# Performance work log

Measured on AMD Instinct MI355X. Metric: run time of the kernel, lower is better.

Reference implementation:

```python
import jax, jax.numpy as jnp
import numpy as np

N_KERNELS = 11
INV_SQRT_2PI = 1.0 / np.sqrt(2.0 * 3.141592653589793)


def kernel_mus(n_kernels):
    l_mu = [1.0]
    if n_kernels == 1:
        return l_mu
    bin_size = 2.0 / (n_kernels - 1)
    l_mu.append(1 - bin_size / 2)
    for i in range(1, n_kernels - 1):
        l_mu.append(l_mu[i] - bin_size)
    return l_mu


def kernel_sigmas(n_kernels):
    bin_size = 2.0 / (n_kernels - 1)
    l_sigma = [0.0001]
    if n_kernels == 1:
        return l_sigma
    l_sigma += [0.5 * bin_size] * (n_kernels - 1)
    return l_sigma


MU = jnp.asarray(kernel_mus(N_KERNELS), dtype=jnp.float32)        # [K]
SIGMA = jnp.asarray(kernel_sigmas(N_KERNELS), dtype=jnp.float32)  # [K]


def setup_inputs() -> dict:
    key = jax.random.key(0)
    k1, k2, k3, k4 = jax.random.split(key, 4)
    B, Q, D, V, E = 512, 32, 256, 32000, 128
    return {
        "query_tokens": jax.random.randint(k1, (B, Q), 0, V),
        "doc_tokens": jax.random.randint(k2, (B, D), 0, V),
        "embedding": jax.random.normal(k3, (V, E), dtype=jnp.float32),
        "fc_weight": jax.random.normal(k4, (1, N_KERNELS), dtype=jnp.float32) * 0.3,
    }


def reference(query_tokens, doc_tokens, embedding, fc_weight):
    # embedding lookup + L2 normalization along feature dim
    q_emb = embedding[query_tokens]                                  # [B,Q,E]
    d_emb = embedding[doc_tokens]                                    # [B,D,E]
    q_n = q_emb / jnp.linalg.norm(q_emb, axis=-1, keepdims=True)
    d_n = d_emb / jnp.linalg.norm(d_emb, axis=-1, keepdims=True)

    # cosine similarity translation matrix [B,Q,D]
    tm = jnp.einsum("bqe,bde->bqd", q_n, d_n)

    # Gaussian kernel responses [B,Q,D,K] (vectorized over kernels)
    diff = tm[..., None] - MU                                        # [B,Q,D,K]
    kmat = jnp.exp(-(diff * diff) / (2.0 * SIGMA * SIGMA)) * INV_SQRT_2PI

    # masking: pad/OOV tokens (id 0) masked out
    q_mask = (query_tokens > 0).astype(jnp.float32)                  # [B,Q]
    d_mask = (doc_tokens > 0).astype(jnp.float32)                    # [B,D]
    kmat = kmat * q_mask[:, :, None, None] * d_mask[:, None, :, None]

    # kernel pooling: sum over doc, log, masked sum over query
    per_kernel_query = jnp.sum(kmat, axis=2)                         # [B,Q,K]
    log_pool = jnp.log(jnp.clip(per_kernel_query, 1e-10)) * q_mask[:, :, None]
    per_kernel = jnp.sum(log_pool, axis=1)                           # [B,K]

    # final linear (no bias) -> score per (query, document) pair
    return jnp.squeeze(per_kernel @ fc_weight.T, axis=-1)            # [B]
```

## Files before the change

### kernel.cpp

```cpp
#include <hip/hip_runtime.h>
#include <hip/hip_bf16.h>

#define EDIM  128
#define QN    32
#define DN    256
#define NK    11

typedef __attribute__((ext_vector_type(8))) short bf16x8;
typedef __attribute__((ext_vector_type(4))) float f32x4;

#define EXP2F(x) __builtin_amdgcn_exp2f(x)

template <int CTRL>
static __device__ inline float dpp_add(float x) {
    int y = __builtin_amdgcn_update_dpp(0, __float_as_int(x), CTRL, 0xF, 0xF, true);
    return x + __int_as_float(y);
}
static __device__ inline float sum16(float x) {
    x = dpp_add<0xB1>(x);
    x = dpp_add<0x4E>(x);
    x = dpp_add<0x124>(x);
    x = dpp_add<0x128>(x);
    return x;
}

static __device__ inline int swz(int r, int c) { return c ^ ((r & 7) << 4); }

static __device__ inline bf16x8 pack8(float4 a, float4 b) {
    union { bf16x8 v; __hip_bfloat16 h[8]; } u;
    u.h[0] = __float2bfloat16(a.x); u.h[1] = __float2bfloat16(a.y);
    u.h[2] = __float2bfloat16(a.z); u.h[3] = __float2bfloat16(a.w);
    u.h[4] = __float2bfloat16(b.x); u.h[5] = __float2bfloat16(b.y);
    u.h[6] = __float2bfloat16(b.z); u.h[7] = __float2bfloat16(b.w);
    return u.v;
}
static __device__ inline float sumsq8(float4 a, float4 b) {
    float s = a.x * a.x + a.y * a.y + a.z * a.z + a.w * a.w;
    s = fmaf(b.x, b.x, s); s = fmaf(b.y, b.y, s);
    s = fmaf(b.z, b.z, s); s = fmaf(b.w, b.w, s);
    return s;
}

__global__ __launch_bounds__(512, 4) void knrm_fused(const int* __restrict__ qtok,
                                                     const int* __restrict__ dtok,
                                                     const float* __restrict__ emb,
                                                     const float* __restrict__ fcw,
                                                     float* __restrict__ out) {
    __shared__ __align__(16) unsigned short dbuf[DN * EDIM];
    __shared__ __align__(16) unsigned short qbuf[QN * EDIM];
    __shared__ float redS[8];

    const float C0 = 0.3989422804014327f;
    const float C1 = 7.30620157e-3f;
    const float C2 = 2.45119242e-6f;
    const float C3 = 1.50605972e-11f;
    const float C4 = 1.69484929e-18f;

    int b = blockIdx.x, tid = threadIdx.x;
    int w = tid >> 6, lane = tid & 63;
    int lr = lane & 15, lg = lane >> 4;
    int qt = w & 1, ds = w >> 1;

    const int* qtb = qtok + b * QN;
    const int* dtb = dtok + b * DN;

    int tq = qtb[(w << 2) + lg];
    int tdA[4], tdB[4];
    #pragma unroll
    for (int it = 0; it < 4; ++it) {
        tdA[it] = dtb[(w << 4) + (it << 2) + lg];
        tdB[it] = dtb[128 + (w << 4) + (it << 2) + lg];
    }
    int tcurs[4], qtr[4];
    #pragma unroll
    for (int t = 0; t < 4; ++t) tcurs[t] = dtb[(t << 6) + (ds << 4) + lr];
    #pragma unroll
    for (int r = 0; r < 4; ++r) qtr[r] = qtb[(qt << 4) + (lg << 2) + r];

    const float4* qsrc = (const float4*)(emb + (size_t)tq * EDIM) + lr * 2;
    float4 qv0 = qsrc[0], qv1 = qsrc[1];
    float4 av[4][2], bv[4][2];
    #pragma unroll
    for (int it = 0; it < 4; ++it) {
        const float4* s0 = (const float4*)(emb + (size_t)tdA[it] * EDIM) + lr * 2;
        av[it][0] = s0[0]; av[it][1] = s0[1];
    }
    #pragma unroll
    for (int it = 0; it < 4; ++it) {
        const float4* s1 = (const float4*)(emb + (size_t)tdB[it] * EDIM) + lr * 2;
        bv[it][0] = s1[0]; bv[it][1] = s1[1];
    }

    {
        int qr = (w << 2) + lg;
        float inv = 1.0f / sqrtf(sum16(sumsq8(qv0, qv1)));
        qv0.x *= inv; qv0.y *= inv; qv0.z *= inv; qv0.w *= inv;
        qv1.x *= inv; qv1.y *= inv; qv1.z *= inv; qv1.w *= inv;
        *(bf16x8*)((char*)qbuf + qr * 256 + swz(qr, lr * 16)) = pack8(qv0, qv1);
    }
    #pragma unroll
    for (int it = 0; it < 4; ++it) {
        int r = (w << 4) + (it << 2) + lg;
        float inv = 1.0f / sqrtf(sum16(sumsq8(av[it][0], av[it][1])));
        float4 v0 = av[it][0], v1 = av[it][1];
        v0.x *= inv; v0.y *= inv; v0.z *= inv; v0.w *= inv;
        v1.x *= inv; v1.y *= inv; v1.z *= inv; v1.w *= inv;
        *(bf16x8*)((char*)dbuf + r * 256 + swz(r, lr * 16)) = pack8(v0, v1);
    }
    #pragma unroll
    for (int it = 0; it < 4; ++it) {
        int r = 128 + (w << 4) + (it << 2) + lg;
        float inv = 1.0f / sqrtf(sum16(sumsq8(bv[it][0], bv[it][1])));
        float4 v0 = bv[it][0], v1 = bv[it][1];
        v0.x *= inv; v0.y *= inv; v0.z *= inv; v0.w *= inv;
        v1.x *= inv; v1.y *= inv; v1.z *= inv; v1.w *= inv;
        *(bf16x8*)((char*)dbuf + r * 256 + swz(r, lr * 16)) = pack8(v0, v1);
    }
    __syncthreads();

    bf16x8 A0, A1, A2, A3;
    {
        int qr = (qt << 4) + lr;
        const char* qb = (const char*)qbuf + qr * 256;
        A0 = *(const bf16x8*)(qb + swz(qr, lg * 16));
        A1 = *(const bf16x8*)(qb + swz(qr, lg * 16 + 64));
        A2 = *(const bf16x8*)(qb + swz(qr, lg * 16 + 128));
        A3 = *(const bf16x8*)(qb + swz(qr, lg * 16 + 192));
    }

    float kacc[4][NK];
    #pragma unroll
    for (int r = 0; r < 4; ++r)
        #pragma unroll
        for (int k = 0; k < NK; ++k) kacc[r][k] = 0.0f;

    #pragma unroll
    for (int t = 0; t < 4; ++t) {
        int dr = (t << 6) + (ds << 4) + lr;
        const char* db = (const char*)dbuf + dr * 256;
        bf16x8 B0 = *(const bf16x8*)(db + swz(dr, lg * 16));
        bf16x8 B1 = *(const bf16x8*)(db + swz(dr, lg * 16 + 64));
        bf16x8 B2 = *(const bf16x8*)(db + swz(dr, lg * 16 + 128));
        bf16x8 B3 = *(const bf16x8*)(db + swz(dr, lg * 16 + 192));
        int tcur = tcurs[t];

        f32x4 acc = {0.0f, 0.0f, 0.0f, 0.0f};
        acc = __builtin_amdgcn_mfma_f32_16x16x32_bf16(A0, B0, acc, 0, 0, 0);
        acc = __builtin_amdgcn_mfma_f32_16x16x32_bf16(A1, B1, acc, 0, 0, 0);
        acc = __builtin_amdgcn_mfma_f32_16x16x32_bf16(A2, B2, acc, 0, 0, 0);
        acc = __builtin_amdgcn_mfma_f32_16x16x32_bf16(A3, B3, acc, 0, 0, 0);

        bool dok = (tcur > 0);
        float mc = dok ? C0 : 0.0f;
        #pragma unroll
        for (int r = 0; r < 4; ++r) {
            float t2 = acc[r];
            kacc[r][0] += (tcur == qtr[r]) ? mc : 0.0f;
            float d  = t2 - 0.1f;
            float g  = EXP2F(d * d * -72.1347520f);
            g = dok ? g : 0.0f;
            float Em = EXP2F(t2 * -28.8539008f);
            float Ep = EXP2F(t2 *  28.8539008f);
            float h = g;
            kacc[r][5]  += h * C0;
            h *= Em; kacc[r][6]  += h * C0;
            h *= Em; kacc[r][7]  += h * C1;
            h *= Em; kacc[r][8]  += h * C2;
            h *= Em; kacc[r][9]  += h * C3;
            h *= Em; kacc[r][10] += h * C4;
            h = g;
            h *= Ep; kacc[r][4]  += h * C1;
            h *= Ep; kacc[r][3]  += h * C2;
            h *= Ep; kacc[r][2]  += h * C3;
            h *= Ep; kacc[r][1]  += h * C4;
        }
    }

    __syncthreads();
    float* part = (float*)qbuf;
    #pragma unroll
    for (int r = 0; r < 4; ++r)
        #pragma unroll
        for (int k = 0; k < NK; ++k) kacc[r][k] = sum16(kacc[r][k]);
    if (lr == 0) {
        float* pw = part + w * (16 * NK) + (lg << 2) * NK;
        #pragma unroll
        for (int r = 0; r < 4; ++r)
            #pragma unroll
            for (int k = 0; k < NK; ++k)
                pw[r * NK + k] = kacc[r][k];
    }
    __syncthreads();

    float total = 0.0f;
    if (tid < QN * NK) {
        int q = tid / NK, k = tid - (tid / NK) * NK;
        int qt2 = q >> 4, row = q & 15;
        const float* pb = part + qt2 * (16 * NK) + row * NK + k;
        float v = pb[0] + pb[2 * 16 * NK] + pb[4 * 16 * NK] + pb[6 * 16 * NK];
        float m = (qtb[q] > 0) ? 1.0f : 0.0f;
        total = m * fcw[k] * __logf(fmaxf(v, 1e-10f));
    }
    #pragma unroll
    for (int off = 32; off; off >>= 1) total += __shfl_xor(total, off);
    if (lane == 0) redS[w] = total;
    __syncthreads();
    if (tid == 0) {
        float s = 0.0f;
        #pragma unroll
        for (int i = 0; i < 8; ++i) s += redS[i];
        out[b] = s;
    }
}

extern "C" void kernel_launch(void* const* d_in, const int* in_sizes, int n_in,
                              void* d_out, int out_size, void* d_ws, size_t ws_size,
                              hipStream_t stream) {
    const int*   qtok = (const int*)d_in[0];
    const int*   dtok = (const int*)d_in[1];
    const float* emb  = (const float*)d_in[2];
    const float* fcw  = (const float*)d_in[3];
    float* out = (float*)d_out;

    int B = in_sizes[0] / QN;
    knrm_fused<<<B, 512, 0, stream>>>(qtok, dtok, emb, fcw, out);
}
```

Baseline: 21.86 us.

## Stream document embeddings in 64-row chunks with prefetch to cut LDS use

Replaces the single 256-row document staging buffer with a 64-row LDS chunk that is refilled four times. The next chunk's embedding rows are loaded from global memory into registers while the current chunk runs MFMA and kernel-pooling math. This shrinks LDS per block and overlaps gather latency with compute. The cost is extra block-wide barriers per chunk and a more serialized fill/compute sequence.

Measured after the change: 21.37 us. 2.2% less time.

```diff
diff --git a/kernel.cpp b/kernel.cpp
--- a/kernel.cpp
+++ b/kernel.cpp
@@ -5,6 +5,7 @@
 #define QN    32
 #define DN    256
 #define NK    11
+#define CHR   64
 
 typedef __attribute__((ext_vector_type(8))) short bf16x8;
 typedef __attribute__((ext_vector_type(4))) float f32x4;
@@ -46,7 +47,7 @@
                                                      const float* __restrict__ emb,
                                                      const float* __restrict__ fcw,
                                                      float* __restrict__ out) {
-    __shared__ __align__(16) unsigned short dbuf[DN * EDIM];
+    __shared__ __align__(16) unsigned short dbuf[CHR * EDIM];
     __shared__ __align__(16) unsigned short qbuf[QN * EDIM];
     __shared__ float redS[8];
 
@@ -65,30 +66,25 @@
     const int* dtb = dtok + b * DN;
 
     int tq = qtb[(w << 2) + lg];
-    int tdA[4], tdB[4];
-    #pragma unroll
-    for (int it = 0; it < 4; ++it) {
-        tdA[it] = dtb[(w << 4) + (it << 2) + lg];
-        tdB[it] = dtb[128 + (w << 4) + (it << 2) + lg];
-    }
+    int td[4][2];
+    #pragma unroll
+    for (int c = 0; c < 4; ++c)
+        #pragma unroll
+        for (int it = 0; it < 2; ++it)
+            td[c][it] = dtb[c * CHR + (w << 3) + (it << 2) + lg];
     int tcurs[4], qtr[4];
     #pragma unroll
-    for (int t = 0; t < 4; ++t) tcurs[t] = dtb[(t << 6) + (ds << 4) + lr];
+    for (int c = 0; c < 4; ++c) tcurs[c] = dtb[c * CHR + (ds << 4) + lr];
     #pragma unroll
     for (int r = 0; r < 4; ++r) qtr[r] = qtb[(qt << 4) + (lg << 2) + r];
 
     const float4* qsrc = (const float4*)(emb + (size_t)tq * EDIM) + lr * 2;
     float4 qv0 = qsrc[0], qv1 = qsrc[1];
-    float4 av[4][2], bv[4][2];
-    #pragma unroll
-    for (int it = 0; it < 4; ++it) {
-        const float4* s0 = (const float4*)(emb + (size_t)tdA[it] * EDIM) + lr * 2;
-        av[it][0] = s0[0]; av[it][1] = s0[1];
-    }
-    #pragma unroll
-    for (int it = 0; it < 4; ++it) {
-        const float4* s1 = (const float4*)(emb + (size_t)tdB[it] * EDIM) + lr * 2;
-        bv[it][0] = s1[0]; bv[it][1] = s1[1];
+    float4 ca[2][2];
+    #pragma unroll
+    for (int it = 0; it < 2; ++it) {
+        const float4* s0 = (const float4*)(emb + (size_t)td[0][it] * EDIM) + lr * 2;
+        ca[it][0] = s0[0]; ca[it][1] = s0[1];
     }
 
     {
@@ -99,22 +95,13 @@
         *(bf16x8*)((char*)qbuf + qr * 256 + swz(qr, lr * 16)) = pack8(qv0, qv1);
     }
     #pragma unroll
-    for (int it = 0; it < 4; ++it) {
-        int r = (w << 4) + (it << 2) + lg;
-        float inv = 1.0f / sqrtf(sum16(sumsq8(av[it][0], av[it][1])));
-        float4 v0 = av[it][0], v1 = av[it][1];
+    for (int it = 0; it < 2; ++it) {
+        int rl = (w << 3) + (it << 2) + lg;
+        float inv = 1.0f / sqrtf(sum16(sumsq8(ca[it][0], ca[it][1])));
+        float4 v0 = ca[it][0], v1 = ca[it][1];
         v0.x *= inv; v0.y *= inv; v0.z *= inv; v0.w *= inv;
         v1.x *= inv; v1.y *= inv; v1.z *= inv; v1.w *= inv;
-        *(bf16x8*)((char*)dbuf + r * 256 + swz(r, lr * 16)) = pack8(v0, v1);
-    }
-    #pragma unroll
-    for (int it = 0; it < 4; ++it) {
-        int r = 128 + (w << 4) + (it << 2) + lg;
-        float inv = 1.0f / sqrtf(sum16(sumsq8(bv[it][0], bv[it][1])));
-        float4 v0 = bv[it][0], v1 = bv[it][1];
-        v0.x *= inv; v0.y *= inv; v0.z *= inv; v0.w *= inv;
-        v1.x *= inv; v1.y *= inv; v1.z *= inv; v1.w *= inv;
-        *(bf16x8*)((char*)dbuf + r * 256 + swz(r, lr * 16)) = pack8(v0, v1);
+        *(bf16x8*)((char*)dbuf + rl * 256 + swz(rl, lr * 16)) = pack8(v0, v1);
     }
     __syncthreads();
 
@@ -135,49 +122,73 @@
         for (int k = 0; k < NK; ++k) kacc[r][k] = 0.0f;
 
     #pragma unroll
-    for (int t = 0; t < 4; ++t) {
-        int dr = (t << 6) + (ds << 4) + lr;
-        const char* db = (const char*)dbuf + dr * 256;
-        bf16x8 B0 = *(const bf16x8*)(db + swz(dr, lg * 16));
-        bf16x8 B1 = *(const bf16x8*)(db + swz(dr, lg * 16 + 64));
-        bf16x8 B2 = *(const bf16x8*)(db + swz(dr, lg * 16 + 128));
-        bf16x8 B3 = *(const bf16x8*)(db + swz(dr, lg * 16 + 192));
-        int tcur = tcurs[t];
-
-        f32x4 acc = {0.0f, 0.0f, 0.0f, 0.0f};
-        acc = __builtin_amdgcn_mfma_f32_16x16x32_bf16(A0, B0, acc, 0, 0, 0);
-        acc = __builtin_amdgcn_mfma_f32_16x16x32_bf16(A1, B1, acc, 0, 0, 0);
-        acc = __builtin_amdgcn_mfma_f32_16x16x32_bf16(A2, B2, acc, 0, 0, 0);
-        acc = __builtin_amdgcn_mfma_f32_16x16x32_bf16(A3, B3, acc, 0, 0, 0);
-
-        bool dok = (tcur > 0);
-        float mc = dok ? C0 : 0.0f;
-        #pragma unroll
-        for (int r = 0; r < 4; ++r) {
-            float t2 = acc[r];
-            kacc[r][0] += (tcur == qtr[r]) ? mc : 0.0f;
-            float d  = t2 - 0.1f;
-            float g  = EXP2F(d * d * -72.1347520f);
-            g = dok ? g : 0.0f;
-            float Em = EXP2F(t2 * -28.8539008f);
-            float Ep = EXP2F(t2 *  28.8539008f);
-            float h = g;
-            kacc[r][5]  += h * C0;
-            h *= Em; kacc[r][6]  += h * C0;
-            h *= Em; kacc[r][7]  += h * C1;
-            h *= Em; kacc[r][8]  += h * C2;
-            h *= Em; kacc[r][9]  += h * C3;
-            h *= Em; kacc[r][10] += h * C4;
-            h = g;
-            h *= Ep; kacc[r][4]  += h * C1;
-            h *= Ep; kacc[r][3]  += h * C2;
-            h *= Ep; kacc[r][2]  += h * C3;
-            h *= Ep; kacc[r][1]  += h * C4;
+    for (int c = 0; c < 4; ++c) {
+        float4 cb[2][2];
+        if (c < 3) {
+            #pragma unroll
+            for (int it = 0; it < 2; ++it) {
+                const float4* s0 = (const float4*)(emb + (size_t)td[c + 1][it] * EDIM) + lr * 2;
+                cb[it][0] = s0[0]; cb[it][1] = s0[1];
+            }
         }
-    }
-
-    __syncthreads();
-    float* part = (float*)qbuf;
+
+        {
+            int rl = (ds << 4) + lr;
+            const char* db = (const char*)dbuf + rl * 256;
+            bf16x8 B0 = *(const bf16x8*)(db + swz(rl, lg * 16));
+            bf16x8 B1 = *(const bf16x8*)(db + swz(rl, lg * 16 + 64));
+            bf16x8 B2 = *(const bf16x8*)(db + swz(rl, lg * 16 + 128));
+            bf16x8 B3 = *(const bf16x8*)(db + swz(rl, lg * 16 + 192));
+            int tcur = tcurs[c];
+
+            f32x4 acc = {0.0f, 0.0f, 0.0f, 0.0f};
+            acc = __builtin_amdgcn_mfma_f32_16x16x32_bf16(A0, B0, acc, 0, 0, 0);
+            acc = __builtin_amdgcn_mfma_f32_16x16x32_bf16(A1, B1, acc, 0, 0, 0);
+            acc = __builtin_amdgcn_mfma_f32_16x16x32_bf16(A2, B2, acc, 0, 0, 0);
+            acc = __builtin_amdgcn_mfma_f32_16x16x32_bf16(A3, B3, acc, 0, 0, 0);
+
+            bool dok = (tcur > 0);
+            float mc = dok ? C0 : 0.0f;
+            #pragma unroll
+            for (int r = 0; r < 4; ++r) {
+                float t2 = acc[r];
+                kacc[r][0] += (tcur == qtr[r]) ? mc : 0.0f;
+                float d  = t2 - 0.1f;
+                float g  = EXP2F(d * d * -72.1347520f);
+                g = dok ? g : 0.0f;
+                float Em = EXP2F(t2 * -28.8539008f);
+                float Ep = EXP2F(t2 *  28.8539008f);
+                float h = g;
+                kacc[r][5]  += h * C0;
+                h *= Em; kacc[r][6]  += h * C0;
+                h *= Em; kacc[r][7]  += h * C1;
+                h *= Em; kacc[r][8]  += h * C2;
+                h *= Em; kacc[r][9]  += h * C3;
+                h *= Em; kacc[r][10] += h * C4;
+                h = g;
+                h *= Ep; kacc[r][4]  += h * C1;
+                h *= Ep; kacc[r][3]  += h * C2;
+                h *= Ep; kacc[r][2]  += h * C3;
+                h *= Ep; kacc[r][1]  += h * C4;
+            }
+        }
+        __syncthreads();
+
+        if (c < 3) {
+            #pragma unroll
+            for (int it = 0; it < 2; ++it) {
+                int rl = (w << 3) + (it << 2) + lg;
+                float inv = 1.0f / sqrtf(sum16(sumsq8(cb[it][0], cb[it][1])));
+                float4 v0 = cb[it][0], v1 = cb[it][1];
+                v0.x *= inv; v0.y *= inv; v0.z *= inv; v0.w *= inv;
+                v1.x *= inv; v1.y *= inv; v1.z *= inv; v1.w *= inv;
+                *(bf16x8*)((char*)dbuf + rl * 256 + swz(rl, lr * 16)) = pack8(v0, v1);
+            }
+            __syncthreads();
+        }
+    }
+
+    float* part = (float*)dbuf;
     #pragma unroll
     for (int r = 0; r < 4; ++r)
         #pragma unroll
```

## Precompute normalized bf16 embedding table in a prepass kernel before main fused kernel

Applied to the files above, without the earlier changes.

Adds a prepass kernel that L2-normalizes the whole 32000x128 fp32 embedding table and writes it to workspace as bf16. The main kernel then gathers half-size bf16 rows with no per-row norm computation. It also replaces the 16-lane DPP reduction with a 4-lane one and writes more partials to shared memory, which the final pass sums. The cost is normalizing and writing the whole vocabulary (16MB read, 8MB write) every call, even though only about 147K rows are gathered, plus a second launch.

Result: slower. 25.35 us (+16.0%).

```diff
diff --git a/kernel.cpp b/kernel.cpp
--- a/kernel.cpp
+++ b/kernel.cpp
@@ -1,6 +1,7 @@
 #include <hip/hip_runtime.h>
 #include <hip/hip_bf16.h>
 
+#define VOCAB 32000
 #define EDIM  128
 #define QN    32
 #define DN    256
@@ -11,41 +12,38 @@
 
 #define EXP2F(x) __builtin_amdgcn_exp2f(x)
 
+static __device__ inline unsigned short f2bf(float f) {
+    unsigned u = __float_as_uint(f);
+    return (unsigned short)((u + 0x7fff + ((u >> 16) & 1)) >> 16);
+}
+
+__global__ __launch_bounds__(256) void norm_bf16_kernel(const float* __restrict__ emb,
+                                                        unsigned int* __restrict__ nbf) {
+    int lane = threadIdx.x & 63;
+    int row  = blockIdx.x * 4 + (threadIdx.x >> 6);
+    const float2* p = (const float2*)(emb + (size_t)row * EDIM);
+    float2 v = p[lane];
+    float s = v.x * v.x + v.y * v.y;
+    #pragma unroll
+    for (int off = 32; off; off >>= 1) s += __shfl_xor(s, off);
+    float inv = 1.0f / sqrtf(s);
+    unsigned int packed = ((unsigned)f2bf(v.y * inv) << 16) | f2bf(v.x * inv);
+    nbf[(size_t)row * (EDIM / 2) + lane] = packed;
+}
+
 template <int CTRL>
 static __device__ inline float dpp_add(float x) {
     int y = __builtin_amdgcn_update_dpp(0, __float_as_int(x), CTRL, 0xF, 0xF, true);
     return x + __int_as_float(y);
 }
-static __device__ inline float sum16(float x) {
-    x = dpp_add<0xB1>(x);
-    x = dpp_add<0x4E>(x);
-    x = dpp_add<0x124>(x);
-    x = dpp_add<0x128>(x);
-    return x;
-}
 
 static __device__ inline int swz(int r, int c) { return c ^ ((r & 7) << 4); }
 
-static __device__ inline bf16x8 pack8(float4 a, float4 b) {
-    union { bf16x8 v; __hip_bfloat16 h[8]; } u;
-    u.h[0] = __float2bfloat16(a.x); u.h[1] = __float2bfloat16(a.y);
-    u.h[2] = __float2bfloat16(a.z); u.h[3] = __float2bfloat16(a.w);
-    u.h[4] = __float2bfloat16(b.x); u.h[5] = __float2bfloat16(b.y);
-    u.h[6] = __float2bfloat16(b.z); u.h[7] = __float2bfloat16(b.w);
-    return u.v;
-}
-static __device__ inline float sumsq8(float4 a, float4 b) {
-    float s = a.x * a.x + a.y * a.y + a.z * a.z + a.w * a.w;
-    s = fmaf(b.x, b.x, s); s = fmaf(b.y, b.y, s);
-    s = fmaf(b.z, b.z, s); s = fmaf(b.w, b.w, s);
-    return s;
-}
-
-__global__ __launch_bounds__(512, 4) void knrm_fused(const int* __restrict__ qtok,
-                                                     const int* __restrict__ dtok,
-                                                     const float* __restrict__ emb,
-                                                     const float* __restrict__ fcw,
-                                                     float* __restrict__ out) {
+__global__ __launch_bounds__(512, 4) void knrm_main(const int* __restrict__ qtok,
+                                                    const int* __restrict__ dtok,
+                                                    const unsigned short* __restrict__ nbf,
+                                                    const float* __restrict__ fcw,
+                                                    float* __restrict__ out) {
     __shared__ __align__(16) unsigned short dbuf[DN * EDIM];
     __shared__ __align__(16) unsigned short qbuf[QN * EDIM];
     __shared__ float redS[8];
@@ -65,56 +63,29 @@
     const int* dtb = dtok + b * DN;
 
     int tq = qtb[(w << 2) + lg];
-    int tdA[4], tdB[4];
-    #pragma unroll
-    for (int it = 0; it < 4; ++it) {
-        tdA[it] = dtb[(w << 4) + (it << 2) + lg];
-        tdB[it] = dtb[128 + (w << 4) + (it << 2) + lg];
-    }
+    int tdr[8];
+    #pragma unroll
+    for (int it = 0; it < 8; ++it) tdr[it] = dtb[(w << 5) + (it << 2) + lg];
     int tcurs[4], qtr[4];
     #pragma unroll
     for (int t = 0; t < 4; ++t) tcurs[t] = dtb[(t << 6) + (ds << 4) + lr];
     #pragma unroll
     for (int r = 0; r < 4; ++r) qtr[r] = qtb[(qt << 4) + (lg << 2) + r];
 
-    const float4* qsrc = (const float4*)(emb + (size_t)tq * EDIM) + lr * 2;
-    float4 qv0 = qsrc[0], qv1 = qsrc[1];
-    float4 av[4][2], bv[4][2];
-    #pragma unroll
-    for (int it = 0; it < 4; ++it) {
-        const float4* s0 = (const float4*)(emb + (size_t)tdA[it] * EDIM) + lr * 2;
-        av[it][0] = s0[0]; av[it][1] = s0[1];
-    }
-    #pragma unroll
-    for (int it = 0; it < 4; ++it) {
-        const float4* s1 = (const float4*)(emb + (size_t)tdB[it] * EDIM) + lr * 2;
-        bv[it][0] = s1[0]; bv[it][1] = s1[1];
-    }
+    bf16x8 qv = *(const bf16x8*)(nbf + (size_t)tq * EDIM + lr * 8);
+    bf16x8 dv[8];
+    #pragma unroll
+    for (int it = 0; it < 8; ++it)
+        dv[it] = *(const bf16x8*)(nbf + (size_t)tdr[it] * EDIM + lr * 8);
 
     {
         int qr = (w << 2) + lg;
-        float inv = 1.0f / sqrtf(sum16(sumsq8(qv0, qv1)));
-        qv0.x *= inv; qv0.y *= inv; qv0.z *= inv; qv0.w *= inv;
-        qv1.x *= inv; qv1.y *= inv; qv1.z *= inv; qv1.w *= inv;
-        *(bf16x8*)((char*)qbuf + qr * 256 + swz(qr, lr * 16)) = pack8(qv0, qv1);
-    }
-    #pragma unroll
-    for (int it = 0; it < 4; ++it) {
-        int r = (w << 4) + (it << 2) + lg;
-        float inv = 1.0f / sqrtf(sum16(sumsq8(av[it][0], av[it][1])));
-        float4 v0 = av[it][0], v1 = av[it][1];
-        v0.x *= inv; v0.y *= inv; v0.z *= inv; v0.w *= inv;
-        v1.x *= inv; v1.y *= inv; v1.z *= inv; v1.w *= inv;
-        *(bf16x8*)((char*)dbuf + r * 256 + swz(r, lr * 16)) = pack8(v0, v1);
-    }
-    #pragma unroll
-    for (int it = 0; it < 4; ++it) {
-        int r = 128 + (w << 4) + (it << 2) + lg;
-        float inv = 1.0f / sqrtf(sum16(sumsq8(bv[it][0], bv[it][1])));
-        float4 v0 = bv[it][0], v1 = bv[it][1];
-        v0.x *= inv; v0.y *= inv; v0.z *= inv; v0.w *= inv;
-        v1.x *= inv; v1.y *= inv; v1.z *= inv; v1.w *= inv;
-        *(bf16x8*)((char*)dbuf + r * 256 + swz(r, lr * 16)) = pack8(v0, v1);
+        *(bf16x8*)((char*)qbuf + qr * 256 + swz(qr, lr * 16)) = qv;
+    }
+    #pragma unroll
+    for (int it = 0; it < 8; ++it) {
+        int r = (w << 5) + (it << 2) + lg;
+        *(bf16x8*)((char*)dbuf + r * 256 + swz(r, lr * 16)) = dv[it];
     }
     __syncthreads();
 
@@ -175,20 +146,31 @@
             h *= Ep; kacc[r][1]  += h * C4;
         }
     }
-
-    __syncthreads();
-    float* part = (float*)qbuf;
+    __syncthreads();
+
     #pragma unroll
     for (int r = 0; r < 4; ++r)
         #pragma unroll
-        for (int k = 0; k < NK; ++k) kacc[r][k] = sum16(kacc[r][k]);
-    if (lr == 0) {
-        float* pw = part + w * (16 * NK) + (lg << 2) * NK;
+        for (int k = 0; k < NK; ++k) {
+            float x = kacc[r][k];
+            x = dpp_add<0xB1>(x);
+            x = dpp_add<0x4E>(x);
+            kacc[r][k] = x;
+        }
+    float* part4 = (float*)dbuf;
+    if ((lr & 3) == 0) {
+        int quad = lr >> 2;
+        float* pw = part4 + (((w << 2) + lg) * 4 + quad) * 48;
+        float flat[44];
         #pragma unroll
         for (int r = 0; r < 4; ++r)
             #pragma unroll
-            for (int k = 0; k < NK; ++k)
-                pw[r * NK + k] = kacc[r][k];
+            for (int k = 0; k < NK; ++k) flat[r * NK + k] = kacc[r][k];
+        #pragma unroll
+        for (int j = 0; j < 11; ++j) {
+            float4 v = {flat[j * 4], flat[j * 4 + 1], flat[j * 4 + 2], flat[j * 4 + 3]};
+            *(float4*)(pw + j * 4) = v;
+        }
     }
     __syncthreads();
 
@@ -196,8 +178,13 @@
     if (tid < QN * NK) {
         int q = tid / NK, k = tid - (tid / NK) * NK;
         int qt2 = q >> 4, row = q & 15;
-        const float* pb = part + qt2 * (16 * NK) + row * NK + k;
-        float v = pb[0] + pb[2 * 16 * NK] + pb[4 * 16 * NK] + pb[6 * 16 * NK];
+        int lg2 = row >> 2, r = row & 3;
+        float v = 0.0f;
+        #pragma unroll
+        for (int d2 = 0; d2 < 4; ++d2)
+            #pragma unroll
+            for (int qd = 0; qd < 4; ++qd)
+                v += part4[((((d2 * 2 + qt2) << 2) + lg2) * 4 + qd) * 48 + r * NK + k];
         float m = (qtb[q] > 0) ? 1.0f : 0.0f;
         total = m * fcw[k] * __logf(fmaxf(v, 1e-10f));
     }
@@ -221,7 +208,10 @@
     const float* emb  = (const float*)d_in[2];
     const float* fcw  = (const float*)d_in[3];
     float* out = (float*)d_out;
+    unsigned int* nbf = (unsigned int*)d_ws;
+
+    norm_bf16_kernel<<<VOCAB / 4, 256, 0, stream>>>(emb, nbf);
 
     int B = in_sizes[0] / QN;
-    knrm_fused<<<B, 512, 0, stream>>>(qtok, dtok, emb, fcw, out);
-}
+    knrm_main<<<B, 512, 0, stream>>>(qtok, dtok, (const unsigned short*)nbf, fcw, out);
+}
```
